# Optimization experiments

Hardware: AMD Instinct MI355X
Metric: run time of the kernel (lower is better)

Reference implementation:

```python
import jax, jax.numpy as jnp
import numpy as np

RES = 32
HEADS = 16
EMB = 1024
DIM_HEAD = EMB // HEADS
BATCH = 8
N = RES * RES
SCALE = DIM_HEAD ** -0.5


def _make_bias_idxs():
    # replicate the LeViT-style |dx|,|dy| offset indexing from __init__
    points = [(i, j) for i in range(RES) for j in range(RES)]
    offsets = {}
    idxs = []
    for p1 in points:
        for p2 in points:
            off = (abs(p1[0] - p2[0]), abs(p1[1] - p2[1]))
            if off not in offsets:
                offsets[off] = len(offsets)
            idxs.append(offsets[off])
    return np.asarray(idxs, dtype=np.int32).reshape(N, N), len(offsets)


def setup_inputs() -> dict:
    key = jax.random.key(0)
    k_x, k_qkv, k_b, k_o = jax.random.split(key, 4)
    bias_idxs, n_off = _make_bias_idxs()  # n_off == 1024 for a 32x32 grid
    return {
        "x": jax.random.normal(k_x, (BATCH, N, EMB), dtype=jnp.float32),
        "W_qkv": jax.random.normal(k_qkv, (3 * EMB, EMB), dtype=jnp.float32) * 0.02,
        "attention_biases": jax.random.normal(k_b, (HEADS, n_off), dtype=jnp.float32) * 0.02,
        "bias_idxs": jnp.asarray(bias_idxs),
        "W_out": jax.random.normal(k_o, (EMB, EMB), dtype=jnp.float32) * 0.02,
        "b_out": jnp.zeros((EMB,), dtype=jnp.float32),
    }


def reference(x, W_qkv, attention_biases, bias_idxs, W_out, b_out):
    B, n, E = x.shape
    # to_qkv: Linear(E, 3E, bias=False) -> x @ W^T
    qkv = x @ W_qkv.T  # [B, n, 3E]
    q, k, v = jnp.split(qkv, 3, axis=-1)

    def heads(t):  # b n (h d) -> b h n d
        return t.reshape(B, n, HEADS, DIM_HEAD).transpose(0, 2, 1, 3)

    q, k, v = heads(q), heads(k), heads(v)
    qk = jnp.einsum("bhnd,bhmd->bhnm", q, k) * SCALE  # [B, h, n, n]
    bias = attention_biases[:, bias_idxs]  # gather -> [h, n, n]
    qk = qk + bias[None]
    attn = jax.nn.softmax(qk, axis=-1)
    out = jnp.einsum("bhnm,bhmd->bhnd", attn, v)
    out = out.transpose(0, 2, 1, 3).reshape(B, n, E)  # b h n d -> b n (h d)
    # to_out: Linear(E, E) with bias (dropout p=0 is identity)
    return out @ W_out.T + b_out
```

## Files before the change

### kernel.cpp

```cpp
#include <hip/hip_runtime.h>

typedef __attribute__((ext_vector_type(8))) short bf16x8;
typedef __attribute__((ext_vector_type(4))) short bf16x4;
typedef __attribute__((ext_vector_type(4))) float f32x4;

#define L2E 1.44269504088896340736f
#define QSCL 0.18033688011112042f

__device__ inline unsigned short f2bf(float f) {
  union { float f; unsigned int u; } x; x.f = f;
  return (unsigned short)((x.u + 0x8000u) >> 16);
}
__device__ inline unsigned int f2bf2(float a, float b) {
  union { float f; unsigned int u; } xa, xb;
  xa.f = a; xb.f = b;
  return ((xa.u + 0x8000u) >> 16) | (((xb.u + 0x8000u) & 0xFFFF0000u));
}
__device__ inline unsigned int pk_bf16(float a, float b) {
#if __has_builtin(__builtin_amdgcn_cvt_pk_bf16_f32)
  typedef __attribute__((ext_vector_type(2))) __bf16 bfv2;
  union { bfv2 v; unsigned int u; } x;
  x.v = __builtin_amdgcn_cvt_pk_bf16_f32(a, b);
  return x.u;
#else
  return f2bf2(a, b);
#endif
}

__device__ inline void gl_lds16(const void* g, void* l) {
  __builtin_amdgcn_global_load_lds((const __attribute__((address_space(1))) void*)g,
                                   (__attribute__((address_space(3))) void*)l,
                                   16, 0, 0);
}

__device__ inline void vm_drain() {
  asm volatile("s_waitcnt vmcnt(0)" ::: "memory");
}

#define N4_X  2097152
#define N4_WQ 786432
#define N4_WO 262144
__global__ void cast3_kernel(const float* __restrict__ x,
                             const float* __restrict__ wq,
                             const float* __restrict__ wo,
                             unsigned short* __restrict__ xb,
                             unsigned short* __restrict__ wqb,
                             unsigned short* __restrict__ wob) {
  int i = blockIdx.x * blockDim.x + threadIdx.x;
  int st = gridDim.x * blockDim.x;
  for (; i < N4_X + N4_WQ + N4_WO; i += st) {
    const float* src; unsigned short* dst; int j;
    if (i < N4_X)            { src = x;  dst = xb;  j = i; }
    else if (i < N4_X + N4_WQ){ src = wq; dst = wqb; j = i - N4_X; }
    else                     { src = wo; dst = wob; j = i - N4_X - N4_WQ; }
    float4 v = reinterpret_cast<const float4*>(src)[j];
    ushort4 o;
    o.x = f2bf(v.x); o.y = f2bf(v.y); o.z = f2bf(v.z); o.w = f2bf(v.w);
    reinterpret_cast<ushort4*>(dst)[j] = o;
  }
}

template <int MODE>
__global__ __launch_bounds__(256, 4) void gemm_qkv_t(
    const unsigned short* __restrict__ A,
    const unsigned short* __restrict__ Bm,
    unsigned short* __restrict__ qo,
    unsigned short* __restrict__ ko,
    unsigned short* __restrict__ vo) {
  __shared__ unsigned short sA[2][128 * 32];
  __shared__ unsigned short sB[2][128 * 32];
  const int K = 1024;
  const int tid = threadIdx.x;
  const int w = tid >> 6, lane = tid & 63;
  const int l15 = lane & 15, quad = lane >> 4;
  const int wm = (w >> 1) * 64, wn = (w & 1) * 64;
  const int tm = blockIdx.y;
  const int tn = (MODE == 0) ? blockIdx.x : blockIdx.x + 16;

  const unsigned short* Ab = A + (size_t)(tm * 128) * K;
  const unsigned short* Bb = Bm + (size_t)(tn * 128) * K;

  const int srow = w * 32 + (lane >> 2);
  const int scol = (((lane & 3) ^ ((lane >> 3) & 3))) * 8;
  const int rsw = (l15 >> 1) & 3;

  const f32x4 fz = {0.f, 0.f, 0.f, 0.f};
  f32x4 acc[4][4];
#pragma unroll
  for (int i = 0; i < 4; i++)
#pragma unroll
    for (int j = 0; j < 4; j++) acc[i][j] = fz;

  gl_lds16(Ab + (size_t)srow * K + scol,        &sA[0][(w * 32) * 32]);
  gl_lds16(Ab + (size_t)(srow + 16) * K + scol, &sA[0][(w * 32 + 16) * 32]);
  gl_lds16(Bb + (size_t)srow * K + scol,        &sB[0][(w * 32) * 32]);
  gl_lds16(Bb + (size_t)(srow + 16) * K + scol, &sB[0][(w * 32 + 16) * 32]);

  int buf = 0;
  for (int k0 = 0; k0 < K; k0 += 32) {
    vm_drain();
    __syncthreads();
    if (k0 + 32 < K) {
      int nb = buf ^ 1, kn = k0 + 32;
      gl_lds16(Ab + (size_t)srow * K + kn + scol,        &sA[nb][(w * 32) * 32]);
      gl_lds16(Ab + (size_t)(srow + 16) * K + kn + scol, &sA[nb][(w * 32 + 16) * 32]);
      gl_lds16(Bb + (size_t)srow * K + kn + scol,        &sB[nb][(w * 32) * 32]);
      gl_lds16(Bb + (size_t)(srow + 16) * K + kn + scol, &sB[nb][(w * 32 + 16) * 32]);
    }
    bf16x8 af[4], bfr[4];
#pragma unroll
    for (int mt = 0; mt < 4; mt++)
      af[mt] = *(const bf16x8*)&sA[buf][(wm + mt * 16 + l15) * 32 + ((quad ^ rsw) << 3)];
#pragma unroll
    for (int nt = 0; nt < 4; nt++)
      bfr[nt] = *(const bf16x8*)&sB[buf][(wn + nt * 16 + l15) * 32 + ((quad ^ rsw) << 3)];
#pragma unroll
    for (int mt = 0; mt < 4; mt++)
#pragma unroll
      for (int nt = 0; nt < 4; nt++) {
        if (MODE == 0)
          acc[mt][nt] = __builtin_amdgcn_mfma_f32_16x16x32_bf16(bfr[nt], af[mt], acc[mt][nt], 0, 0, 0);
        else
          acc[mt][nt] = __builtin_amdgcn_mfma_f32_16x16x32_bf16(af[mt], bfr[nt], acc[mt][nt], 0, 0, 0);
      }
    buf ^= 1;
  }

  const int m0 = tm * 128;
  const int bb = m0 >> 10, n0 = m0 & 1023;
  const int cbase = (tn * 128) & 1023;

  if (MODE == 0) {
    const int which = tn >> 3;
    const float scl = (which == 0) ? QSCL : 1.0f;
    unsigned short* dst = (which == 0) ? qo : ko;
#pragma unroll
    for (int mt = 0; mt < 4; mt++) {
      int tok = n0 + wm + mt * 16 + l15;
#pragma unroll
      for (int nt = 0; nt < 4; nt++) {
        int c = cbase + wn + nt * 16 + quad * 4;
        int hh = c >> 6, d0 = c & 63;
        uint2 val;
        val.x = f2bf2(acc[mt][nt][0] * scl, acc[mt][nt][1] * scl);
        val.y = f2bf2(acc[mt][nt][2] * scl, acc[mt][nt][3] * scl);
        *(uint2*)&dst[(((size_t)bb * 16 + hh) * 1024 + tok) * 64 + d0] = val;
      }
    }
  } else {
#pragma unroll
    for (int mt = 0; mt < 4; mt++) {
      int tok = n0 + wm + mt * 16 + quad * 4;
#pragma unroll
      for (int nt = 0; nt < 4; nt++) {
        int c = cbase + wn + nt * 16 + l15;
        int hh = c >> 6, dd = c & 63;
        uint2 val;
        val.x = f2bf2(acc[mt][nt][0], acc[mt][nt][1]);
        val.y = f2bf2(acc[mt][nt][2], acc[mt][nt][3]);
        *(uint2*)&vo[(((size_t)bb * 16 + hh) * 64 + dd) * 1024 + tok] = val;
      }
    }
  }
}

__global__ __launch_bounds__(256, 4) void attn_kernel(
    const unsigned short* __restrict__ Q,
    const unsigned short* __restrict__ Kg,
    const unsigned short* __restrict__ Vt,
    const float* __restrict__ biases,
    unsigned short* __restrict__ Og) {
  __shared__ unsigned short sK[2][64 * 64];
  __shared__ unsigned short sV[2][64 * 64];
  __shared__ float sBias2[32 * 63];

  const int bx = blockIdx.x;
  const int bh = bx & 127, qt = bx >> 7;
  const int h = bh & 15, b = bh >> 4;
  const int tid = threadIdx.x, w = tid >> 6, lane = tid & 63;
  const int l15 = lane & 15, quad = lane >> 4;

  const size_t bhs = (size_t)(b * 16 + h);
  const unsigned short* qbase = Q + (bhs * 1024 + (size_t)qt * 128) * 64;
  const unsigned short* kbase = Kg + bhs * 1024 * 64;
  const unsigned short* vbase = Vt + bhs * 64 * 1024;

  for (int t = tid; t < 2048; t += 256) {
    int d = t >> 6, u = t & 63;
    if (u < 63) {
      int dj = u - 31; dj = dj < 0 ? -dj : dj;
      sBias2[d * 63 + u] = biases[h * 1024 + d * 32 + dj] * L2E;
    }
  }

  const int sr0 = w * 16 + (lane >> 3);
  const int sc8 = lane & 7;
  const int sw0 = sc8 ^ (lane >> 3);

  gl_lds16(kbase + (size_t)sr0 * 64 + sw0 * 8,        &sK[0][(w * 16) * 64]);
  gl_lds16(kbase + (size_t)(sr0 + 8) * 64 + sw0 * 8,  &sK[0][(w * 16 + 8) * 64]);
  gl_lds16(vbase + (size_t)sr0 * 1024 + sw0 * 8,      &sV[0][(w * 16) * 64]);
  gl_lds16(vbase + (size_t)(sr0 + 8) * 1024 + sw0 * 8,&sV[0][(w * 16 + 8) * 64]);

  bf16x8 qf[2][2];
#pragma unroll
  for (int qb = 0; qb < 2; qb++)
#pragma unroll
    for (int kd = 0; kd < 2; kd++)
      qf[qb][kd] = *(const bf16x8*)(qbase + (w * 32 + qb * 16 + l15) * 64 + kd * 32 + quad * 8);

  const int qg0 = qt * 128 + w * 32;
  const int qiw = __builtin_amdgcn_readfirstlane(qt * 4 + w);
  int cc[2][2];
#pragma unroll
  for (int qb = 0; qb < 2; qb++)
#pragma unroll
    for (int kp = 0; kp < 2; kp++)
      cc[qb][kp] = qb * 16 + l15 - kp * 16 - quad * 4;

  const f32x4 fz = {0.f, 0.f, 0.f, 0.f};
  f32x4 of[2][4], osum[2];
#pragma unroll
  for (int i = 0; i < 2; i++) {
    osum[i] = fz;
#pragma unroll
    for (int j = 0; j < 4; j++) of[i][j] = fz;
  }
  const bf16x4 vones = {(short)0x3F80, (short)0x3F80, (short)0x3F80, (short)0x3F80};

  int buf = 0;
  for (int j0 = 0; j0 < 1024; j0 += 64) {
    vm_drain();
    __syncthreads();
    if (j0 + 64 < 1024) {
      int nb = buf ^ 1, jn = j0 + 64;
      gl_lds16(kbase + (size_t)(jn + sr0) * 64 + sw0 * 8,       &sK[nb][(w * 16) * 64]);
      gl_lds16(kbase + (size_t)(jn + sr0 + 8) * 64 + sw0 * 8,   &sK[nb][(w * 16 + 8) * 64]);
      gl_lds16(vbase + (size_t)sr0 * 1024 + jn + sw0 * 8,       &sV[nb][(w * 16) * 64]);
      gl_lds16(vbase + (size_t)(sr0 + 8) * 1024 + jn + sw0 * 8, &sV[nb][(w * 16 + 8) * 64]);
    }
    const unsigned short* K_ = sK[buf];
    const unsigned short* V_ = sV[buf];
    const int j5 = j0 >> 5;
    const int dh = qiw - j5;
    const float* bA = sBias2 + abs(dh) * 63 + 31;
    const float* bB = sBias2 + abs(dh - 1) * 63 + 31;

#pragma unroll
    for (int kvb = 0; kvb < 4; kvb++) {
      bf16x8 kf0 = *(const bf16x8*)&K_[(kvb * 16 + l15) * 64 + ((quad ^ (l15 & 7)) << 3)];
      bf16x8 kf1 = *(const bf16x8*)&K_[(kvb * 16 + l15) * 64 + (((4 + quad) ^ (l15 & 7)) << 3)];
      bf16x4 vf[4];
#pragma unroll
      for (int nt = 0; nt < 4; nt++) {
        int d = nt * 16 + l15;
        vf[nt] = *(const bf16x4*)&V_[d * 64 + (((kvb * 2 + (quad >> 1)) ^ (l15 & 7)) << 3) + (quad & 1) * 4];
      }
      const float* bp = (kvb < 2) ? bA : bB;
      const int kp = kvb & 1;
#pragma unroll
      for (int qb = 0; qb < 2; qb++) {
        f32x4 s4 = __builtin_amdgcn_mfma_f32_16x16x32_bf16(kf0, qf[qb][0], fz, 0, 0, 0);
        s4 = __builtin_amdgcn_mfma_f32_16x16x32_bf16(kf1, qf[qb][1], s4, 0, 0, 0);
        const float* bq = bp + cc[qb][kp];
        float p0 = __builtin_amdgcn_exp2f(s4.x + bq[0]);
        float p1 = __builtin_amdgcn_exp2f(s4.y + bq[-1]);
        float p2 = __builtin_amdgcn_exp2f(s4.z + bq[-2]);
        float p3 = __builtin_amdgcn_exp2f(s4.w + bq[-3]);
        union { unsigned int u[2]; bf16x4 v; } pk;
        pk.u[0] = pk_bf16(p0, p1);
        pk.u[1] = pk_bf16(p2, p3);
#pragma unroll
        for (int nt = 0; nt < 4; nt++)
          of[qb][nt] = __builtin_amdgcn_mfma_f32_16x16x16bf16_1k(pk.v, vf[nt], of[qb][nt], 0, 0, 0);
        osum[qb] = __builtin_amdgcn_mfma_f32_16x16x16bf16_1k(pk.v, vones, osum[qb], 0, 0, 0);
      }
    }
    buf ^= 1;
  }

  const int kvq = quad * 4;
#pragma unroll
  for (int qb = 0; qb < 2; qb++)
#pragma unroll
    for (int r = 0; r < 4; r++) {
      float inv = __builtin_amdgcn_rcpf(osum[qb][r]);
      int n = qg0 + qb * 16 + kvq + r;
      size_t orow = ((size_t)b * 1024 + n) * 1024 + h * 64;
#pragma unroll
      for (int nt = 0; nt < 4; nt++)
        Og[orow + nt * 16 + l15] = f2bf(of[qb][nt][r] * inv);
    }
}

__global__ __launch_bounds__(256, 4) void gemm_out_k(
    const unsigned short* __restrict__ A,
    const unsigned short* __restrict__ Bm,
    const float* __restrict__ bias,
    float* __restrict__ out) {
  __shared__ unsigned short sA[2][128 * 32];
  __shared__ unsigned short sB[2][128 * 32];
  const int K = 1024;
  const int tid = threadIdx.x;
  const int w = tid >> 6, lane = tid & 63;
  const int l15 = lane & 15, quad = lane >> 4;
  const int wm = (w >> 1) * 64, wn = (w & 1) * 64;
  const int tm = blockIdx.y, tn = blockIdx.x;

  const unsigned short* Ab = A + (size_t)(tm * 128) * K;
  const unsigned short* Bb = Bm + (size_t)(tn * 128) * K;

  const int srow = w * 32 + (lane >> 2);
  const int scol = (((lane & 3) ^ ((lane >> 3) & 3))) * 8;
  const int rsw = (l15 >> 1) & 3;

  const f32x4 fz = {0.f, 0.f, 0.f, 0.f};
  f32x4 acc[4][4];
#pragma unroll
  for (int i = 0; i < 4; i++)
#pragma unroll
    for (int j = 0; j < 4; j++) acc[i][j] = fz;

  gl_lds16(Ab + (size_t)srow * K + scol,        &sA[0][(w * 32) * 32]);
  gl_lds16(Ab + (size_t)(srow + 16) * K + scol, &sA[0][(w * 32 + 16) * 32]);
  gl_lds16(Bb + (size_t)srow * K + scol,        &sB[0][(w * 32) * 32]);
  gl_lds16(Bb + (size_t)(srow + 16) * K + scol, &sB[0][(w * 32 + 16) * 32]);

  int buf = 0;
  for (int k0 = 0; k0 < K; k0 += 32) {
    vm_drain();
    __syncthreads();
    if (k0 + 32 < K) {
      int nb = buf ^ 1, kn = k0 + 32;
      gl_lds16(Ab + (size_t)srow * K + kn + scol,        &sA[nb][(w * 32) * 32]);
      gl_lds16(Ab + (size_t)(srow + 16) * K + kn + scol, &sA[nb][(w * 32 + 16) * 32]);
      gl_lds16(Bb + (size_t)srow * K + kn + scol,        &sB[nb][(w * 32) * 32]);
      gl_lds16(Bb + (size_t)(srow + 16) * K + kn + scol, &sB[nb][(w * 32 + 16) * 32]);
    }
    bf16x8 af[4], bfr[4];
#pragma unroll
    for (int mt = 0; mt < 4; mt++)
      af[mt] = *(const bf16x8*)&sA[buf][(wm + mt * 16 + l15) * 32 + ((quad ^ rsw) << 3)];
#pragma unroll
    for (int nt = 0; nt < 4; nt++)
      bfr[nt] = *(const bf16x8*)&sB[buf][(wn + nt * 16 + l15) * 32 + ((quad ^ rsw) << 3)];
#pragma unroll
    for (int mt = 0; mt < 4; mt++)
#pragma unroll
      for (int nt = 0; nt < 4; nt++)
        acc[mt][nt] = __builtin_amdgcn_mfma_f32_16x16x32_bf16(af[mt], bfr[nt], acc[mt][nt], 0, 0, 0);
    buf ^= 1;
  }

  const int m0 = tm * 128 + wm, c0 = tn * 128 + wn;
#pragma unroll
  for (int mt = 0; mt < 4; mt++)
#pragma unroll
    for (int nt = 0; nt < 4; nt++)
#pragma unroll
      for (int r = 0; r < 4; r++) {
        int m = m0 + mt * 16 + quad * 4 + r;
        int c = c0 + nt * 16 + l15;
        out[(size_t)m * 1024 + c] = acc[mt][nt][r] + bias[c];
      }
}

extern "C" void kernel_launch(void* const* d_in, const int* in_sizes, int n_in,
                              void* d_out, int out_size, void* d_ws, size_t ws_size,
                              hipStream_t stream) {
  const float* x    = (const float*)d_in[0];
  const float* Wqkv = (const float*)d_in[1];
  const float* ab   = (const float*)d_in[2];
  const float* Wout = (const float*)d_in[4];
  const float* bout = (const float*)d_in[5];
  float* out = (float*)d_out;

  char* ws = (char*)d_ws;
  unsigned short* xb  = (unsigned short*)(ws);
  unsigned short* wqb = (unsigned short*)(ws + 16777216);
  unsigned short* wob = (unsigned short*)(ws + 23068672);
  unsigned short* qw  = (unsigned short*)(ws + 25165824);
  unsigned short* kw  = (unsigned short*)(ws + 41943040);
  unsigned short* vw  = (unsigned short*)(ws + 58720256);
  unsigned short* ow  = (unsigned short*)(ws + 75497472);

  cast3_kernel<<<1536, 256, 0, stream>>>(x, Wqkv, Wout, xb, wqb, wob);
  gemm_qkv_t<0><<<dim3(16, 64), 256, 0, stream>>>(xb, wqb, qw, kw, vw);
  gemm_qkv_t<1><<<dim3(8, 64), 256, 0, stream>>>(xb, wqb, qw, kw, vw);
  attn_kernel<<<1024, 256, 0, stream>>>(qw, kw, vw, ab, ow);
  gemm_out_k<<<dim3(8, 64), 256, 0, stream>>>(ow, wob, bout, out);
}
```

Measured before the change: 264.8 us.

## Merge QKV GEMM launches and double attention query rows per wave

The two QKV GEMM launches become one 24-column grid that picks the Q/K or V mode per block, which removes a launch and the tail between them. The attention kernel now gives each wave 64 query rows instead of 32, halving the grid to 512 blocks. Each K/V tile loaded into LDS therefore serves twice as many queries, and the bias lookup gains a third row pointer for the second 32-row group. In exchange the larger accumulator set raises register pressure, launch bounds drop to 2 blocks per CU, and fewer blocks are available to fill the GPU.

```diff
diff --git a/kernel.cpp b/kernel.cpp
--- a/kernel.cpp
+++ b/kernel.cpp
@@ -61,7 +61,110 @@
 }
 
 template <int MODE>
-__global__ __launch_bounds__(256, 4) void gemm_qkv_t(
+__device__ __forceinline__ void gemm_qkv_body(
+    unsigned short* __restrict__ sA,
+    unsigned short* __restrict__ sB,
+    const unsigned short* __restrict__ A,
+    const unsigned short* __restrict__ Bm,
+    unsigned short* __restrict__ qo,
+    unsigned short* __restrict__ ko,
+    unsigned short* __restrict__ vo) {
+  const int K = 1024;
+  const int tid = threadIdx.x;
+  const int w = tid >> 6, lane = tid & 63;
+  const int l15 = lane & 15, quad = lane >> 4;
+  const int wm = (w >> 1) * 64, wn = (w & 1) * 64;
+  const int tm = blockIdx.y;
+  const int tn = blockIdx.x;
+
+  const unsigned short* Ab = A + (size_t)(tm * 128) * K;
+  const unsigned short* Bb = Bm + (size_t)(tn * 128) * K;
+
+  const int srow = w * 32 + (lane >> 2);
+  const int scol = (((lane & 3) ^ ((lane >> 3) & 3))) * 8;
+  const int rsw = (l15 >> 1) & 3;
+
+  const f32x4 fz = {0.f, 0.f, 0.f, 0.f};
+  f32x4 acc[4][4];
+#pragma unroll
+  for (int i = 0; i < 4; i++)
+#pragma unroll
+    for (int j = 0; j < 4; j++) acc[i][j] = fz;
+
+  gl_lds16(Ab + (size_t)srow * K + scol,        &sA[(w * 32) * 32]);
+  gl_lds16(Ab + (size_t)(srow + 16) * K + scol, &sA[(w * 32 + 16) * 32]);
+  gl_lds16(Bb + (size_t)srow * K + scol,        &sB[(w * 32) * 32]);
+  gl_lds16(Bb + (size_t)(srow + 16) * K + scol, &sB[(w * 32 + 16) * 32]);
+
+  int buf = 0;
+  for (int k0 = 0; k0 < K; k0 += 32) {
+    vm_drain();
+    __syncthreads();
+    if (k0 + 32 < K) {
+      int nb = buf ^ 1, kn = k0 + 32;
+      gl_lds16(Ab + (size_t)srow * K + kn + scol,        &sA[nb * 4096 + (w * 32) * 32]);
+      gl_lds16(Ab + (size_t)(srow + 16) * K + kn + scol, &sA[nb * 4096 + (w * 32 + 16) * 32]);
+      gl_lds16(Bb + (size_t)srow * K + kn + scol,        &sB[nb * 4096 + (w * 32) * 32]);
+      gl_lds16(Bb + (size_t)(srow + 16) * K + kn + scol, &sB[nb * 4096 + (w * 32 + 16) * 32]);
+    }
+    bf16x8 af[4], bfr[4];
+#pragma unroll
+    for (int mt = 0; mt < 4; mt++)
+      af[mt] = *(const bf16x8*)&sA[buf * 4096 + (wm + mt * 16 + l15) * 32 + ((quad ^ rsw) << 3)];
+#pragma unroll
+    for (int nt = 0; nt < 4; nt++)
+      bfr[nt] = *(const bf16x8*)&sB[buf * 4096 + (wn + nt * 16 + l15) * 32 + ((quad ^ rsw) << 3)];
+#pragma unroll
+    for (int mt = 0; mt < 4; mt++)
+#pragma unroll
+      for (int nt = 0; nt < 4; nt++) {
+        if (MODE == 0)
+          acc[mt][nt] = __builtin_amdgcn_mfma_f32_16x16x32_bf16(bfr[nt], af[mt], acc[mt][nt], 0, 0, 0);
+        else
+          acc[mt][nt] = __builtin_amdgcn_mfma_f32_16x16x32_bf16(af[mt], bfr[nt], acc[mt][nt], 0, 0, 0);
+      }
+    buf ^= 1;
+  }
+
+  const int m0 = tm * 128;
+  const int bb = m0 >> 10, n0 = m0 & 1023;
+  const int cbase = (tn * 128) & 1023;
+
+  if (MODE == 0) {
+    const int which = tn >> 3;
+    const float scl = (which == 0) ? QSCL : 1.0f;
+    unsigned short* dst = (which == 0) ? qo : ko;
+#pragma unroll
+    for (int mt = 0; mt < 4; mt++) {
+      int tok = n0 + wm + mt * 16 + l15;
+#pragma unroll
+      for (int nt = 0; nt < 4; nt++) {
+        int c = cbase + wn + nt * 16 + quad * 4;
+        int hh = c >> 6, d0 = c & 63;
+        uint2 val;
+        val.x = f2bf2(acc[mt][nt][0] * scl, acc[mt][nt][1] * scl);
+        val.y = f2bf2(acc[mt][nt][2] * scl, acc[mt][nt][3] * scl);
+        *(uint2*)&dst[(((size_t)bb * 16 + hh) * 1024 + tok) * 64 + d0] = val;
+      }
+    }
+  } else {
+#pragma unroll
+    for (int mt = 0; mt < 4; mt++) {
+      int tok = n0 + wm + mt * 16 + quad * 4;
+#pragma unroll
+      for (int nt = 0; nt < 4; nt++) {
+        int c = cbase + wn + nt * 16 + l15;
+        int hh = c >> 6, dd = c & 63;
+        uint2 val;
+        val.x = f2bf2(acc[mt][nt][0], acc[mt][nt][1]);
+        val.y = f2bf2(acc[mt][nt][2], acc[mt][nt][3]);
+        *(uint2*)&vo[(((size_t)bb * 16 + hh) * 64 + dd) * 1024 + tok] = val;
+      }
+    }
+  }
+}
+
+__global__ __launch_bounds__(256, 4) void gemm_qkv(
     const unsigned short* __restrict__ A,
     const unsigned short* __restrict__ Bm,
     unsigned short* __restrict__ qo,
@@ -69,102 +172,11 @@
     unsigned short* __restrict__ vo) {
   __shared__ unsigned short sA[2][128 * 32];
   __shared__ unsigned short sB[2][128 * 32];
-  const int K = 1024;
-  const int tid = threadIdx.x;
-  const int w = tid >> 6, lane = tid & 63;
-  const int l15 = lane & 15, quad = lane >> 4;
-  const int wm = (w >> 1) * 64, wn = (w & 1) * 64;
-  const int tm = blockIdx.y;
-  const int tn = (MODE == 0) ? blockIdx.x : blockIdx.x + 16;
-
-  const unsigned short* Ab = A + (size_t)(tm * 128) * K;
-  const unsigned short* Bb = Bm + (size_t)(tn * 128) * K;
-
-  const int srow = w * 32 + (lane >> 2);
-  const int scol = (((lane & 3) ^ ((lane >> 3) & 3))) * 8;
-  const int rsw = (l15 >> 1) & 3;
-
-  const f32x4 fz = {0.f, 0.f, 0.f, 0.f};
-  f32x4 acc[4][4];
-#pragma unroll
-  for (int i = 0; i < 4; i++)
-#pragma unroll
-    for (int j = 0; j < 4; j++) acc[i][j] = fz;
-
-  gl_lds16(Ab + (size_t)srow * K + scol,        &sA[0][(w * 32) * 32]);
-  gl_lds16(Ab + (size_t)(srow + 16) * K + scol, &sA[0][(w * 32 + 16) * 32]);
-  gl_lds16(Bb + (size_t)srow * K + scol,        &sB[0][(w * 32) * 32]);
-  gl_lds16(Bb + (size_t)(srow + 16) * K + scol, &sB[0][(w * 32 + 16) * 32]);
-
-  int buf = 0;
-  for (int k0 = 0; k0 < K; k0 += 32) {
-    vm_drain();
-    __syncthreads();
-    if (k0 + 32 < K) {
-      int nb = buf ^ 1, kn = k0 + 32;
-      gl_lds16(Ab + (size_t)srow * K + kn + scol,        &sA[nb][(w * 32) * 32]);
-      gl_lds16(Ab + (size_t)(srow + 16) * K + kn + scol, &sA[nb][(w * 32 + 16) * 32]);
-      gl_lds16(Bb + (size_t)srow * K + kn + scol,        &sB[nb][(w * 32) * 32]);
-      gl_lds16(Bb + (size_t)(srow + 16) * K + kn + scol, &sB[nb][(w * 32 + 16) * 32]);
-    }
-    bf16x8 af[4], bfr[4];
-#pragma unroll
-    for (int mt = 0; mt < 4; mt++)
-      af[mt] = *(const bf16x8*)&sA[buf][(wm + mt * 16 + l15) * 32 + ((quad ^ rsw) << 3)];
-#pragma unroll
-    for (int nt = 0; nt < 4; nt++)
-      bfr[nt] = *(const bf16x8*)&sB[buf][(wn + nt * 16 + l15) * 32 + ((quad ^ rsw) << 3)];
-#pragma unroll
-    for (int mt = 0; mt < 4; mt++)
-#pragma unroll
-      for (int nt = 0; nt < 4; nt++) {
-        if (MODE == 0)
-          acc[mt][nt] = __builtin_amdgcn_mfma_f32_16x16x32_bf16(bfr[nt], af[mt], acc[mt][nt], 0, 0, 0);
-        else
-          acc[mt][nt] = __builtin_amdgcn_mfma_f32_16x16x32_bf16(af[mt], bfr[nt], acc[mt][nt], 0, 0, 0);
-      }
-    buf ^= 1;
-  }
-
-  const int m0 = tm * 128;
-  const int bb = m0 >> 10, n0 = m0 & 1023;
-  const int cbase = (tn * 128) & 1023;
-
-  if (MODE == 0) {
-    const int which = tn >> 3;
-    const float scl = (which == 0) ? QSCL : 1.0f;
-    unsigned short* dst = (which == 0) ? qo : ko;
-#pragma unroll
-    for (int mt = 0; mt < 4; mt++) {
-      int tok = n0 + wm + mt * 16 + l15;
-#pragma unroll
-      for (int nt = 0; nt < 4; nt++) {
-        int c = cbase + wn + nt * 16 + quad * 4;
-        int hh = c >> 6, d0 = c & 63;
-        uint2 val;
-        val.x = f2bf2(acc[mt][nt][0] * scl, acc[mt][nt][1] * scl);
-        val.y = f2bf2(acc[mt][nt][2] * scl, acc[mt][nt][3] * scl);
-        *(uint2*)&dst[(((size_t)bb * 16 + hh) * 1024 + tok) * 64 + d0] = val;
-      }
-    }
-  } else {
-#pragma unroll
-    for (int mt = 0; mt < 4; mt++) {
-      int tok = n0 + wm + mt * 16 + quad * 4;
-#pragma unroll
-      for (int nt = 0; nt < 4; nt++) {
-        int c = cbase + wn + nt * 16 + l15;
-        int hh = c >> 6, dd = c & 63;
-        uint2 val;
-        val.x = f2bf2(acc[mt][nt][0], acc[mt][nt][1]);
-        val.y = f2bf2(acc[mt][nt][2], acc[mt][nt][3]);
-        *(uint2*)&vo[(((size_t)bb * 16 + hh) * 64 + dd) * 1024 + tok] = val;
-      }
-    }
-  }
-}
-
-__global__ __launch_bounds__(256, 4) void attn_kernel(
+  if (blockIdx.x < 16) gemm_qkv_body<0>(&sA[0][0], &sB[0][0], A, Bm, qo, ko, vo);
+  else                 gemm_qkv_body<1>(&sA[0][0], &sB[0][0], A, Bm, qo, ko, vo);
+}
+
+__global__ __launch_bounds__(256, 2) void attn_kernel(
     const unsigned short* __restrict__ Q,
     const unsigned short* __restrict__ Kg,
     const unsigned short* __restrict__ Vt,
@@ -181,7 +193,7 @@
   const int l15 = lane & 15, quad = lane >> 4;
 
   const size_t bhs = (size_t)(b * 16 + h);
-  const unsigned short* qbase = Q + (bhs * 1024 + (size_t)qt * 128) * 64;
+  const unsigned short* qbase = Q + (bhs * 1024 + (size_t)qt * 256) * 64;
   const unsigned short* kbase = Kg + bhs * 1024 * 64;
   const unsigned short* vbase = Vt + bhs * 64 * 1024;
 
@@ -202,26 +214,26 @@
   gl_lds16(vbase + (size_t)sr0 * 1024 + sw0 * 8,      &sV[0][(w * 16) * 64]);
   gl_lds16(vbase + (size_t)(sr0 + 8) * 1024 + sw0 * 8,&sV[0][(w * 16 + 8) * 64]);
 
-  bf16x8 qf[2][2];
-#pragma unroll
-  for (int qb = 0; qb < 2; qb++)
+  bf16x8 qf[4][2];
+#pragma unroll
+  for (int qb = 0; qb < 4; qb++)
 #pragma unroll
     for (int kd = 0; kd < 2; kd++)
-      qf[qb][kd] = *(const bf16x8*)(qbase + (w * 32 + qb * 16 + l15) * 64 + kd * 32 + quad * 8);
-
-  const int qg0 = qt * 128 + w * 32;
-  const int qiw = __builtin_amdgcn_readfirstlane(qt * 4 + w);
-  int cc[2][2];
-#pragma unroll
-  for (int qb = 0; qb < 2; qb++)
+      qf[qb][kd] = *(const bf16x8*)(qbase + (w * 64 + qb * 16 + l15) * 64 + kd * 32 + quad * 8);
+
+  const int qg0 = qt * 256 + w * 64;
+  const int qtw = __builtin_amdgcn_readfirstlane(qt * 8 + w * 2);
+  int cc2[2][2];
+#pragma unroll
+  for (int qh = 0; qh < 2; qh++)
 #pragma unroll
     for (int kp = 0; kp < 2; kp++)
-      cc[qb][kp] = qb * 16 + l15 - kp * 16 - quad * 4;
+      cc2[qh][kp] = qh * 16 + l15 - kp * 16 - quad * 4;
 
   const f32x4 fz = {0.f, 0.f, 0.f, 0.f};
-  f32x4 of[2][4], osum[2];
-#pragma unroll
-  for (int i = 0; i < 2; i++) {
+  f32x4 of[4][4], osum[4];
+#pragma unroll
+  for (int i = 0; i < 4; i++) {
     osum[i] = fz;
 #pragma unroll
     for (int j = 0; j < 4; j++) of[i][j] = fz;
@@ -242,9 +254,10 @@
     const unsigned short* K_ = sK[buf];
     const unsigned short* V_ = sV[buf];
     const int j5 = j0 >> 5;
-    const int dh = qiw - j5;
-    const float* bA = sBias2 + abs(dh) * 63 + 31;
-    const float* bB = sBias2 + abs(dh - 1) * 63 + 31;
+    const int dh = qtw - j5;
+    const float* b0 = sBias2 + abs(dh) * 63 + 31;
+    const float* bM = sBias2 + abs(dh - 1) * 63 + 31;
+    const float* bP = sBias2 + abs(dh + 1) * 63 + 31;
 
 #pragma unroll
     for (int kvb = 0; kvb < 4; kvb++) {
@@ -256,13 +269,14 @@
         int d = nt * 16 + l15;
         vf[nt] = *(const bf16x4*)&V_[d * 64 + (((kvb * 2 + (quad >> 1)) ^ (l15 & 7)) << 3) + (quad & 1) * 4];
       }
-      const float* bp = (kvb < 2) ? bA : bB;
       const int kp = kvb & 1;
 #pragma unroll
-      for (int qb = 0; qb < 2; qb++) {
+      for (int qb = 0; qb < 4; qb++) {
         f32x4 s4 = __builtin_amdgcn_mfma_f32_16x16x32_bf16(kf0, qf[qb][0], fz, 0, 0, 0);
         s4 = __builtin_amdgcn_mfma_f32_16x16x32_bf16(kf1, qf[qb][1], s4, 0, 0, 0);
-        const float* bq = bp + cc[qb][kp];
+        const float* bp = (qb < 2) ? ((kvb < 2) ? b0 : bM)
+                                   : ((kvb < 2) ? bP : b0);
+        const float* bq = bp + cc2[qb & 1][kp];
         float p0 = __builtin_amdgcn_exp2f(s4.x + bq[0]);
         float p1 = __builtin_amdgcn_exp2f(s4.y + bq[-1]);
         float p2 = __builtin_amdgcn_exp2f(s4.z + bq[-2]);
@@ -281,7 +295,7 @@
 
   const int kvq = quad * 4;
 #pragma unroll
-  for (int qb = 0; qb < 2; qb++)
+  for (int qb = 0; qb < 4; qb++)
 #pragma unroll
     for (int r = 0; r < 4; r++) {
       float inv = __builtin_amdgcn_rcpf(osum[qb][r]);
@@ -385,8 +399,7 @@
   unsigned short* ow  = (unsigned short*)(ws + 75497472);
 
   cast3_kernel<<<1536, 256, 0, stream>>>(x, Wqkv, Wout, xb, wqb, wob);
-  gemm_qkv_t<0><<<dim3(16, 64), 256, 0, stream>>>(xb, wqb, qw, kw, vw);
-  gemm_qkv_t<1><<<dim3(8, 64), 256, 0, stream>>>(xb, wqb, qw, kw, vw);
-  attn_kernel<<<1024, 256, 0, stream>>>(qw, kw, vw, ab, ow);
+  gemm_qkv<<<dim3(24, 64), 256, 0, stream>>>(xb, wqb, qw, kw, vw);
+  attn_kernel<<<512, 256, 0, stream>>>(qw, kw, vw, ab, ow);
   gemm_out_k<<<dim3(8, 64), 256, 0, stream>>>(ow, wob, bout, out);
 }
```

After: 252.7 us. 1.05x faster.
